# Optimization experiments

Hardware: AMD Instinct MI355X
Metric: run time of the kernel (lower is better)

Reference implementation:

```python
import jax, jax.numpy as jnp
import numpy as np

B, T, E, H, HD = 4, 1500, 1280, 20, 64
SCALING = HD ** -0.5


def setup_inputs() -> dict:
    key = jax.random.key(0)
    ks = jax.random.split(key, 8)
    s = 0.02
    return {
        "hidden_states": jax.random.normal(ks[0], (B, 1, T, E), jnp.float32),
        "attention_mask": jnp.zeros((B, 1, T, T), jnp.float32),
        "Wq": jax.random.normal(ks[1], (H, HD, E), jnp.float32) * s,
        "bq": jax.random.normal(ks[2], (H, HD), jnp.float32) * s,
        "Wk": jax.random.normal(ks[3], (H, HD, E), jnp.float32) * s,
        "Wv": jax.random.normal(ks[4], (H, HD, E), jnp.float32) * s,
        "bv": jax.random.normal(ks[5], (H, HD), jnp.float32) * s,
        "Wo": jax.random.normal(ks[6], (E, E), jnp.float32) * s,
        "bo": jax.random.normal(ks[7], (E,), jnp.float32) * s,
    }


def reference(hidden_states, attention_mask, Wq, bq, Wk, Wv, bv, Wo, bo):
    # hidden_states: [B, 1, T, E] (NHWC with H=1, as in the torch module)
    b, _, t, e = hidden_states.shape
    x = hidden_states[:, 0]  # [B, T, E]
    # Per-head 1x1 Conv2d projections == batched linear over stacked head weights.
    # Scaling is folded into q (the module bakes it into q_proj weights/bias).
    q = (jnp.einsum("bte,hde->bhtd", x, Wq) + bq[None, :, None, :]) * SCALING
    k = jnp.einsum("bse,hde->bhsd", x, Wk)
    v = jnp.einsum("bse,hde->bhsd", x, Wv) + bv[None, :, None, :]
    # attention_mask broadcasts over the head dim (module adds it per head as [B,1,T,S])
    scores = jnp.einsum("bhtd,bhsd->bhts", q, k) + attention_mask  # [B,H,T,S]
    attn = jax.nn.softmax(scores, axis=-1)
    out = jnp.einsum("bhts,bhsd->bhtd", attn, v)  # [B,H,T,HD]
    out = out.transpose(0, 2, 1, 3).reshape(b, t, e)  # concat heads on channel dim
    final = jnp.einsum("bte,fe->btf", out, Wo) + bo  # 1x1 Conv2d out_proj
    return final[:, None, :, :]  # [B,1,T,E]
```

## Files before the change

### kernel.cpp

```cpp
#include <hip/hip_runtime.h>

#define T_LEN 1500
#define TP    1536
#define EDIM  1280
#define NH    20
#define HD    64
#define KDIM  1280
#define NT    20

#define LOG2E 1.4426950408889634f

#define OFF_X    ((size_t)0)
#define OFF_AO   ((size_t)0)
#define OFF_W    ((size_t)7700480)
#define OFF_WO   ((size_t)12615680)
#define OFF_Q    ((size_t)14254080)
#define OFF_K    ((size_t)22118400)
#define OFF_VT   ((size_t)29982720)

typedef float  f32x4  __attribute__((ext_vector_type(4)));
typedef float  f32x16 __attribute__((ext_vector_type(16)));
typedef short  s16x8  __attribute__((ext_vector_type(8)));
typedef __bf16 bf16x8 __attribute__((ext_vector_type(8)));
typedef unsigned short u16;
typedef unsigned int   u32;
typedef unsigned int u32x4 __attribute__((ext_vector_type(4)));

__device__ __forceinline__ f32x4 mfma_bf16(s16x8 a, s16x8 b, f32x4 c) {
  return __builtin_amdgcn_mfma_f32_16x16x32_bf16(
      __builtin_bit_cast(bf16x8, a), __builtin_bit_cast(bf16x8, b), c, 0, 0, 0);
}

__device__ __forceinline__ f32x16 mfma32(s16x8 a, s16x8 b, f32x16 c) {
  return __builtin_amdgcn_mfma_f32_32x32x16_bf16(
      __builtin_bit_cast(bf16x8, a), __builtin_bit_cast(bf16x8, b), c, 0, 0, 0);
}

__device__ __forceinline__ u16 f2bf(float f) {
  union { float f; unsigned int u; } a; a.f = f;
  return (u16)((a.u + 0x7fffu + ((a.u >> 16) & 1u)) >> 16);
}

__device__ __forceinline__ float fexp2(float x) {
  return __builtin_amdgcn_exp2f(x);
}

__device__ __forceinline__ void gl_lds16(const u16* g, u16* l) {
  __builtin_amdgcn_global_load_lds(
      (const __attribute__((address_space(1))) unsigned int*)(const void*)g,
      (__attribute__((address_space(3))) unsigned int*)(void*)l, 16, 0, 0);
}


__global__ __launch_bounds__(256) void prep_kernel(
    const float* __restrict__ x, const float* __restrict__ wq,
    const float* __restrict__ wk, const float* __restrict__ wv,
    const float* __restrict__ wo, const float* __restrict__ mask,
    u16* __restrict__ ws, u32* __restrict__ nzflags) {
  const int S0 = 1925120;
  const int S1 = 1228800;
  const int S2 = 409600;
  const int P1 = 46080;
  const int S3 = 2250000;
  const int TOT = S0 + S1 + S2 + 3 * P1 + S3;
  for (int v = blockIdx.x * 256 + threadIdx.x; v < TOT; v += gridDim.x * 256) {
    if (v < S0) {
      int i = v * 4;
      int m = i / EDIM, e = i - m * EDIM;
      int ep = (e & ~63) | (((((e >> 3) & 7) ^ (m & 7))) << 3) | (e & 7);
      ushort4 o;
      if (m < 6000) {
        float4 f = *(const float4*)(x + i);
        o = make_ushort4(f2bf(f.x), f2bf(f.y), f2bf(f.z), f2bf(f.w));
      } else {
        o = make_ushort4(0, 0, 0, 0);
      }
      *(ushort4*)(ws + OFF_X + (size_t)m * EDIM + ep) = o;
    } else if (v < S0 + S1) {
      int j = (v - S0) * 4;
      int n = j / EDIM, e = j - n * EDIM;
      const float* s = (n < 1280) ? wq + (size_t)n * EDIM + e
                     : (n < 2560) ? wk + (size_t)(n - 1280) * EDIM + e
                                  : wv + (size_t)(n - 2560) * EDIM + e;
      float4 f = *(const float4*)s;
      int ep = (e & ~63) | (((((e >> 3) & 7) ^ (n & 7))) << 3) | (e & 7);
      *(ushort4*)(ws + OFF_W + (size_t)n * EDIM + ep) =
          make_ushort4(f2bf(f.x), f2bf(f.y), f2bf(f.z), f2bf(f.w));
    } else if (v < S0 + S1 + S2) {
      int j = (v - S0 - S1) * 4;
      int n = j / EDIM, e = j - n * EDIM;
      float4 f = *(const float4*)(wo + j);
      int ep = (e & ~63) | (((((e >> 3) & 7) ^ (n & 7))) << 3) | (e & 7);
      *(ushort4*)(ws + OFF_WO + (size_t)n * EDIM + ep) =
          make_ushort4(f2bf(f.x), f2bf(f.y), f2bf(f.z), f2bf(f.w));
    } else if (v < S0 + S1 + S2 + 3 * P1) {
      int p = v - (S0 + S1 + S2);
      ushort4 z = make_ushort4(0, 0, 0, 0);
      if (p < P1) {
        int p4 = p * 4; int bh = p4 / 2304; int rem = p4 - bh * 2304;
        int tt = rem >> 6, d = rem & 63;
        *(ushort4*)(ws + OFF_Q + ((size_t)(bh * TP + 1500 + tt)) * HD + d) = z;
      } else if (p < 2 * P1) {
        int p4 = (p - P1) * 4; int bh = p4 / 2304; int rem = p4 - bh * 2304;
        int tt = rem >> 6, d = rem & 63;
        *(ushort4*)(ws + OFF_K + ((size_t)(bh * TP + 1500 + tt)) * HD + d) = z;
      } else {
        int p4 = (p - 2 * P1) * 4; int bh = p4 / 2304; int rem = p4 - bh * 2304;
        int d = rem / 36, ss = rem - d * 36;
        int t = 1500 + ss;
        int tphys = (t & ~63) | (((((t >> 3) & 7) ^ (d & 7))) << 3) | (t & 7);
        *(ushort4*)(ws + OFF_VT + ((size_t)(bh * HD + d)) * TP + tphys) = z;
      }
    } else {
      int p = v - (S0 + S1 + S2 + 3 * P1);
      int i4 = p * 4;
      int bb = i4 / 2250000;
      int rem = i4 - bb * 2250000;
      int q = rem / 1500;
      int s = rem - q * 1500;
      float4 f = *(const float4*)(mask + (size_t)bb * 2250000 + rem);
      if (f.x != 0.f || f.y != 0.f || f.z != 0.f || f.w != 0.f)
        atomicOr(&nzflags[(bb * 12 + (q >> 7)) * 24 + (s >> 6)], 1u);
    }
  }
}

__device__ __forceinline__ void gemm_mainloop256(
    const u16* __restrict__ A, const u16* __restrict__ B,
    int mt, int nt, u16* lds, f32x4 acc[4][4]) {
  const int tid = threadIdx.x;
  const int lane = tid & 63, wid = tid >> 6;
  const int lg = lane >> 4, lr = lane & 15;
  const int wr = wid >> 1, wn = wid & 1;

  const u16* aB = A + (size_t)(mt * 256) * KDIM;
  const u16* bB = B + (size_t)(nt * 128) * KDIM;
  size_t aOff[4], bOff[2];
  #pragma unroll
  for (int l = 0; l < 4; ++l) {
    int gid = l * 512 + tid;
    aOff[l] = (size_t)(gid >> 3) * KDIM + (gid & 7) * 8;
  }
  #pragma unroll
  for (int l = 0; l < 2; ++l) {
    int gid = l * 512 + tid;
    bOff[l] = (size_t)(gid >> 3) * KDIM + (gid & 7) * 8;
  }
  const int ldsOff = tid * 8;
  int arow[4], brow[4];
  #pragma unroll
  for (int i = 0; i < 4; ++i) arow[i] = (wr * 64 + i * 16 + lr) * 64;
  #pragma unroll
  for (int j = 0; j < 4; ++j) brow[j] = (wn * 64 + j * 16 + lr) * 64;
  const int gsw0 = ((lg) ^ (lr & 7)) * 8;
  const int gsw1 = ((4 + lg) ^ (lr & 7)) * 8;

  #pragma unroll
  for (int t = 0; t < 2; ++t) {
    u16* dA = lds + t * 24576;
    u16* dB = dA + 16384;
    gl_lds16(aB + aOff[0] + t * 64, dA + ldsOff);
    gl_lds16(aB + aOff[1] + t * 64, dA + ldsOff + 4096);
    gl_lds16(bB + bOff[0] + t * 64, dB + ldsOff);
    gl_lds16(aB + aOff[2] + t * 64, dA + ldsOff + 8192);
    gl_lds16(aB + aOff[3] + t * 64, dA + ldsOff + 12288);
    gl_lds16(bB + bOff[1] + t * 64, dB + ldsOff + 4096);
  }
  asm volatile("s_waitcnt vmcnt(6)" ::: "memory");
  __builtin_amdgcn_s_barrier();
  __builtin_amdgcn_sched_barrier(0);
  s16x8 ca[4], cb[4];
  #pragma unroll
  for (int i = 0; i < 4; ++i) ca[i] = *(const s16x8*)(lds + arow[i] + gsw0);
  #pragma unroll
  for (int j = 0; j < 4; ++j) cb[j] = *(const s16x8*)(lds + 16384 + brow[j] + gsw0);

  int s = 0;
  #pragma unroll 1
  for (int kt = 0; kt < NT; ++kt) {
    u16* cA = lds + s * 24576;
    u16* cB = cA + 16384;
    int ssl = s + 2; if (ssl >= 3) ssl -= 3;
    u16* sA = lds + ssl * 24576;
    u16* sB = sA + 16384;
    const bool doStage = (kt + 2 < NT);
    if (doStage) {
      gl_lds16(aB + aOff[0] + (kt + 2) * 64, sA + ldsOff);
      gl_lds16(aB + aOff[1] + (kt + 2) * 64, sA + ldsOff + 4096);
      gl_lds16(bB + bOff[0] + (kt + 2) * 64, sB + ldsOff);
    }
    s16x8 na[4], nb[4];
    #pragma unroll
    for (int i = 0; i < 4; ++i) na[i] = *(const s16x8*)(cA + arow[i] + gsw1);
    #pragma unroll
    for (int j = 0; j < 4; ++j) nb[j] = *(const s16x8*)(cB + brow[j] + gsw1);
    __builtin_amdgcn_s_setprio(1);
    #pragma unroll
    for (int i = 0; i < 4; ++i)
      #pragma unroll
      for (int j = 0; j < 4; ++j)
        acc[i][j] = mfma_bf16(ca[i], cb[j], acc[i][j]);
    __builtin_amdgcn_s_setprio(0);
    if (doStage) {
      gl_lds16(aB + aOff[2] + (kt + 2) * 64, sA + ldsOff + 8192);
      gl_lds16(aB + aOff[3] + (kt + 2) * 64, sA + ldsOff + 12288);
      gl_lds16(bB + bOff[1] + (kt + 2) * 64, sB + ldsOff + 4096);
    }
    if (kt < NT - 1) {
      asm volatile("s_waitcnt lgkmcnt(0)" ::: "memory");
      if (kt < NT - 2) asm volatile("s_waitcnt vmcnt(6)" ::: "memory");
      else             asm volatile("s_waitcnt vmcnt(0)" ::: "memory");
      __builtin_amdgcn_s_barrier();
      __builtin_amdgcn_sched_barrier(0);
      int sn = s + 1; if (sn >= 3) sn = 0;
      const u16* nA = lds + sn * 24576;
      const u16* nB2 = nA + 16384;
      #pragma unroll
      for (int i = 0; i < 4; ++i) ca[i] = *(const s16x8*)(nA + arow[i] + gsw0);
      #pragma unroll
      for (int j = 0; j < 4; ++j) cb[j] = *(const s16x8*)(nB2 + brow[j] + gsw0);
    }
    __builtin_amdgcn_s_setprio(1);
    #pragma unroll
    for (int i = 0; i < 4; ++i)
      #pragma unroll
      for (int j = 0; j < 4; ++j)
        acc[i][j] = mfma_bf16(na[i], nb[j], acc[i][j]);
    __builtin_amdgcn_s_setprio(0);
    s = s + 1; if (s >= 3) s = 0;
  }
}

__global__ __launch_bounds__(512) void gemm_qkv_kernel(
    const u16* __restrict__ X, const u16* __restrict__ W,
    const float* __restrict__ bq, const float* __restrict__ bv,
    u16* __restrict__ Qw, u16* __restrict__ Kw, u16* __restrict__ Vtw) {
  __shared__ __align__(16) u16 lds[3 * 24576];
  const int bid = blockIdx.x;
  const int xcd = bid & 7, idx = bid >> 3;
  const int mt = xcd * 3 + idx % 3;
  const int nt = idx / 3;
  f32x4 acc[4][4] = {};
  gemm_mainloop256(X, W, mt, nt, lds, acc);
  const int tid = threadIdx.x;
  const int lane = tid & 63, wid = tid >> 6;
  const int lg = lane >> 4, lr = lane & 15;
  const int wr = wid >> 1, wn = wid & 1;
  #pragma unroll
  for (int i = 0; i < 4; ++i) {
    #pragma unroll
    for (int r = 0; r < 4; ++r) {
      int mm = mt * 256 + wr * 64 + i * 16 + lg * 4 + r;
      if (mm >= 6000) continue;
      int bt = mm / 1500, tt = mm - bt * 1500;
      #pragma unroll
      for (int j = 0; j < 4; ++j) {
        int n = nt * 128 + wn * 64 + j * 16 + lr;
        float v = acc[i][j][r];
        if (n < 1280) {
          int hh = n >> 6, d = n & 63;
          Qw[((size_t)(bt * NH + hh) * TP + tt) * HD + d] =
              f2bf((v + bq[n]) * (0.125f * LOG2E));
        } else if (n < 2560) {
          int nn = n - 1280, hh = nn >> 6, d = nn & 63;
          int dp = ((((d >> 3) ^ (tt & 7))) << 3) | (d & 7);
          Kw[((size_t)(bt * NH + hh) * TP + tt) * HD + dp] = f2bf(v);
        } else {
          int nn = n - 2560, hh = nn >> 6, d = nn & 63;
          int tphys = (tt & ~63) | (((((tt >> 3) & 7) ^ (d & 7))) << 3) | (tt & 7);
          Vtw[((size_t)(bt * NH + hh) * HD + d) * TP + tphys] = f2bf(v + bv[nn]);
        }
      }
    }
  }
}

__global__ __launch_bounds__(256) void attn_kernel(
    const u16* __restrict__ Qw, const u16* __restrict__ Kw,
    const u16* __restrict__ Vtw, const float* __restrict__ mask,
    const u32* __restrict__ nzflags, u16* __restrict__ AO) {
  __shared__ __align__(16) u16 Kb[2][64 * 64];
  __shared__ __align__(16) u16 Vb[2][64 * 64];
  const int bid = blockIdx.x;
  const int qt = bid / 80;
  const int bhid = bid % 80;
  const int bb = bhid / NH, hh = bhid % NH;
  const int tid = threadIdx.x;
  const int w = tid >> 6;
  const int lane = tid & 63;
  const int lq = lane & 31;
  const int hi = lane >> 5;
  const int q0 = qt * 128 + w * 32;
  const int qrow = q0 + lq;
  const int qm = qrow < (T_LEN - 1) ? qrow : (T_LEN - 1);
  const u16* Qp = Qw + (size_t)bhid * TP * HD;
  const u16* Kp = Kw + (size_t)bhid * TP * HD;
  const u16* Vp = Vtw + (size_t)bhid * HD * TP;
  const float* mp = mask + (size_t)bb * T_LEN * T_LEN + (size_t)qm * T_LEN;
  const u32* nzp = nzflags + (bb * 12 + qt) * 24;

  s16x8 qf[4];
  #pragma unroll
  for (int c = 0; c < 4; ++c)
    qf[c] = *(const s16x8*)(Qp + (size_t)qrow * HD + c * 16 + hi * 8);

  s16x8 ones;
  #pragma unroll
  for (int i = 0; i < 8; ++i) ones[i] = (short)0x3F80;

  f32x16 O0 = {}, O1 = {}, lacc = {};
  float m = -3e38f;

  {
    gl_lds16(Kp + tid * 8,                 Kb[0] + tid * 8);
    gl_lds16(Kp + 2048 + tid * 8,          Kb[0] + 2048 + tid * 8);
    int r = tid >> 3, g = tid & 7;
    gl_lds16(Vp + (size_t)r * TP + g * 8,          Vb[0] + tid * 8);
    gl_lds16(Vp + (size_t)(r + 32) * TP + g * 8,   Vb[0] + 2048 + tid * 8);
  }
  __syncthreads();

  int buf = 0;
  #pragma unroll 1
  for (int st = 0; st < 24; ++st) {
    const int s0 = st * 64;
    if (st < 23) {
      const int sn = s0 + 64;
      gl_lds16(Kp + (size_t)sn * HD + tid * 8,        Kb[buf ^ 1] + tid * 8);
      gl_lds16(Kp + (size_t)sn * HD + 2048 + tid * 8, Kb[buf ^ 1] + 2048 + tid * 8);
      int r = tid >> 3, g = tid & 7;
      gl_lds16(Vp + (size_t)r * TP + sn + g * 8,        Vb[buf ^ 1] + tid * 8);
      gl_lds16(Vp + (size_t)(r + 32) * TP + sn + g * 8, Vb[buf ^ 1] + 2048 + tid * 8);
    }
    const bool has_mask = nzp[st] != 0u;
    const u16* kb = Kb[buf];
    f32x16 S0a = {}, S1a = {};
    #pragma unroll
    for (int c = 0; c < 4; ++c) {
      int gc = 2 * c + hi;
      int gs = (gc ^ (lq & 7)) << 3;
      s16x8 k0 = *(const s16x8*)(kb + lq * 64 + gs);
      s16x8 k1 = *(const s16x8*)(kb + (32 + lq) * 64 + gs);
      S0a = mfma32(k0, qf[c], S0a);
      S1a = mfma32(k1, qf[c], S1a);
    }
    float p[32];
    #pragma unroll
    for (int r = 0; r < 16; ++r) { p[r] = S0a[r]; p[16 + r] = S1a[r]; }
    if (has_mask) {
      f32x4 mk[2][4];
      #pragma unroll
      for (int sh = 0; sh < 2; ++sh)
        #pragma unroll
        for (int g = 0; g < 4; ++g) {
          int sb = s0 + sh * 32 + 8 * g + 4 * hi;
          if (sb > T_LEN - 4) sb = T_LEN - 4;
          mk[sh][g] = *(const f32x4*)(mp + sb);
        }
      #pragma unroll
      for (int r = 0; r < 16; ++r) {
        p[r]      = fmaf(mk[0][r >> 2][r & 3], LOG2E, p[r]);
        p[16 + r] = fmaf(mk[1][r >> 2][r & 3], LOG2E, p[16 + r]);
      }
    }
    if (st == 23) {
      if (hi) { p[12] = p[13] = p[14] = p[15] = -1e30f; }
      #pragma unroll
      for (int r = 16; r < 32; ++r) p[r] = -1e30f;
    }
    float t1[16];
    #pragma unroll
    for (int r = 0; r < 16; ++r) t1[r] = fmaxf(p[r], p[r + 16]);
    #pragma unroll
    for (int r = 0; r < 8; ++r) t1[r] = fmaxf(t1[r], t1[r + 8]);
    float mx = fmaxf(fmaxf(fmaxf(t1[0], t1[1]), fmaxf(t1[2], t1[3])),
                     fmaxf(fmaxf(t1[4], t1[5]), fmaxf(t1[6], t1[7])));
    mx = fmaxf(mx, __shfl_xor(mx, 32));
    if (!__all(mx <= m + 8.f)) {
      float mn = fmaxf(m, mx);
      float sc = fexp2(m - mn);
      O0 *= sc; O1 *= sc; lacc *= sc;
      m = mn;
    }
    #pragma unroll
    for (int r = 0; r < 32; ++r) p[r] = fexp2(p[r] - m);
    const u16* vb = Vb[buf];
    #pragma unroll
    for (int sh = 0; sh < 2; ++sh) {
      u32 pk[8];
      #pragma unroll
      for (int j = 0; j < 8; ++j)
        asm("v_cvt_pk_bf16_f32 %0, %1, %2"
            : "=v"(pk[j]) : "v"(p[sh * 16 + 2 * j]), "v"(p[sh * 16 + 2 * j + 1]));
      asm("v_permlane32_swap_b32 %0, %1" : "+v"(pk[0]), "+v"(pk[2]));
      asm("v_permlane32_swap_b32 %0, %1" : "+v"(pk[1]), "+v"(pk[3]));
      asm("v_permlane32_swap_b32 %0, %1" : "+v"(pk[4]), "+v"(pk[6]));
      asm("v_permlane32_swap_b32 %0, %1" : "+v"(pk[5]), "+v"(pk[7]));
      u32x4 ta = {pk[0], pk[1], pk[2], pk[3]};
      u32x4 tb = {pk[4], pk[5], pk[6], pk[7]};
      s16x8 pfa = __builtin_bit_cast(s16x8, ta);
      s16x8 pfb = __builtin_bit_cast(s16x8, tb);
      lacc = mfma32(ones, pfa, lacc);
      lacc = mfma32(ones, pfb, lacc);
      int ga = sh * 4 + hi, gb = sh * 4 + 2 + hi;
      {
        int d = lq;
        s16x8 va = *(const s16x8*)(vb + d * 64 + ((ga ^ (d & 7)) << 3));
        s16x8 vc = *(const s16x8*)(vb + d * 64 + ((gb ^ (d & 7)) << 3));
        O0 = mfma32(va, pfa, O0);
        O0 = mfma32(vc, pfb, O0);
      }
      {
        int d = 32 + lq;
        s16x8 va = *(const s16x8*)(vb + d * 64 + ((ga ^ (d & 7)) << 3));
        s16x8 vc = *(const s16x8*)(vb + d * 64 + ((gb ^ (d & 7)) << 3));
        O1 = mfma32(va, pfa, O1);
        O1 = mfma32(vc, pfb, O1);
      }
    }
    __syncthreads();
    buf ^= 1;
  }

  if (qrow < T_LEN) {
    float inv = 1.f / lacc[0];
    int arow = bb * T_LEN + qrow;
    int key = arow & 7;
    size_t base = (size_t)arow * EDIM + hh * 64;
    #pragma unroll
    for (int g = 0; g < 4; ++g) {
      ushort4 o0, o1;
      o0.x = f2bf(O0[4 * g + 0] * inv); o0.y = f2bf(O0[4 * g + 1] * inv);
      o0.z = f2bf(O0[4 * g + 2] * inv); o0.w = f2bf(O0[4 * g + 3] * inv);
      o1.x = f2bf(O1[4 * g + 0] * inv); o1.y = f2bf(O1[4 * g + 1] * inv);
      o1.z = f2bf(O1[4 * g + 2] * inv); o1.w = f2bf(O1[4 * g + 3] * inv);
      *(ushort4*)(AO + base + ((g ^ key) << 3) + 4 * hi)       = o0;
      *(ushort4*)(AO + base + (((4 + g) ^ key) << 3) + 4 * hi) = o1;
    }
  }
}

__global__ __launch_bounds__(512) void gemm_out_kernel(
    const u16* __restrict__ AOb, const u16* __restrict__ Wob,
    const float* __restrict__ bo, float* __restrict__ out) {
  __shared__ __align__(16) u16 lds[3 * 24576];
  const int bid = blockIdx.x;
  const int xcd = bid & 7, idx = bid >> 3;
  const int mt = xcd * 3 + idx % 3;
  const int nt = idx / 3;
  f32x4 acc[4][4] = {};
  gemm_mainloop256(AOb, Wob, mt, nt, lds, acc);
  const int tid = threadIdx.x;
  const int lane = tid & 63, wid = tid >> 6;
  const int lg = lane >> 4, lr = lane & 15;
  const int wr = wid >> 1, wn = wid & 1;
  #pragma unroll
  for (int i = 0; i < 4; ++i) {
    #pragma unroll
    for (int r = 0; r < 4; ++r) {
      int mm = mt * 256 + wr * 64 + i * 16 + lg * 4 + r;
      if (mm >= 6000) continue;
      #pragma unroll
      for (int j = 0; j < 4; ++j) {
        int n = nt * 128 + wn * 64 + j * 16 + lr;
        out[(size_t)mm * EDIM + n] = acc[i][j][r] + bo[n];
      }
    }
  }
}

extern "C" void kernel_launch(void* const* d_in, const int* in_sizes, int n_in,
                              void* d_out, int out_size, void* d_ws, size_t ws_size,
                              hipStream_t stream) {
  const float* x    = (const float*)d_in[0];
  const float* mask = (const float*)d_in[1];
  const float* wq   = (const float*)d_in[2];
  const float* bq   = (const float*)d_in[3];
  const float* wk   = (const float*)d_in[4];
  const float* wv   = (const float*)d_in[5];
  const float* bv   = (const float*)d_in[6];
  const float* wo   = (const float*)d_in[7];
  const float* bo   = (const float*)d_in[8];
  float* out = (float*)d_out;
  u16* ws = (u16*)d_ws;
  u32* nzflags = (u32*)d_out;

  hipMemsetAsync(nzflags, 0, 1152 * sizeof(u32), stream);
  prep_kernel<<<2048, 256, 0, stream>>>(x, wq, wk, wv, wo, mask, ws, nzflags);
  gemm_qkv_kernel<<<720, 512, 0, stream>>>(
      ws + OFF_X, ws + OFF_W, bq, bv, ws + OFF_Q, ws + OFF_K, ws + OFF_VT);
  attn_kernel<<<960, 256, 0, stream>>>(
      ws + OFF_Q, ws + OFF_K, ws + OFF_VT, mask, nzflags, ws + OFF_AO);
  gemm_out_kernel<<<240, 512, 0, stream>>>(
      ws + OFF_AO, ws + OFF_WO, bo, out);
}
```

Baseline: 242.4 us.

## Use 256x256 square tiles with double-buffered mainloop for QKV GEMM

Replaces the 256x128 triple-buffered QKV GEMM mainloop with a 256x256 tile, 8 waves arranged 2x4, each computing 128x64 with a two-stage LDS double buffer. The grid is halved to 360 blocks, raising arithmetic intensity per loaded byte. The trade-offs are more accumulator registers (128 floats per thread), fewer blocks than CUs (a possible load imbalance), and a shallower prefetch pipeline with a full barrier each k-step.

```diff
diff --git a/kernel.cpp b/kernel.cpp
--- a/kernel.cpp
+++ b/kernel.cpp
@@ -125,6 +125,90 @@
   }
 }
 
+__device__ __forceinline__ void gemm_mainloop256sq(
+    const u16* __restrict__ A, const u16* __restrict__ B,
+    int mt, int nt, u16* lds, f32x4 acc[8][4]) {
+  const int tid = threadIdx.x;
+  const int lane = tid & 63, wid = tid >> 6;
+  const int lg = lane >> 4, lr = lane & 15;
+  const int wr = wid >> 2, wn = wid & 3;
+
+  const u16* aB = A + (size_t)(mt * 256) * KDIM;
+  const u16* bB = B + (size_t)(nt * 256) * KDIM;
+  size_t off[4];
+  #pragma unroll
+  for (int l = 0; l < 4; ++l) {
+    int gid = l * 512 + tid;
+    off[l] = (size_t)(gid >> 3) * KDIM + (gid & 7) * 8;
+  }
+  const int ldsOff = tid * 8;
+  int arow[8], brow[4];
+  #pragma unroll
+  for (int i = 0; i < 8; ++i) arow[i] = (wr * 128 + i * 16 + lr) * 64;
+  #pragma unroll
+  for (int j = 0; j < 4; ++j) brow[j] = 16384 + (wn * 64 + j * 16 + lr) * 64;
+  const int gsw0 = ((lg) ^ (lr & 7)) * 8;
+  const int gsw1 = ((4 + lg) ^ (lr & 7)) * 8;
+
+  #pragma unroll
+  for (int l = 0; l < 4; ++l) gl_lds16(aB + off[l], lds + ldsOff + l * 4096);
+  #pragma unroll
+  for (int l = 0; l < 4; ++l) gl_lds16(bB + off[l], lds + 16384 + ldsOff + l * 4096);
+  asm volatile("s_waitcnt vmcnt(0)" ::: "memory");
+  __builtin_amdgcn_s_barrier();
+  __builtin_amdgcn_sched_barrier(0);
+
+  int s = 0;
+  #pragma unroll 1
+  for (int kt = 0; kt < NT; ++kt) {
+    const u16* cur = lds + s * 32768;
+    u16* nxt = lds + (s ^ 1) * 32768;
+    if (kt + 1 < NT) {
+      #pragma unroll
+      for (int l = 0; l < 4; ++l)
+        gl_lds16(aB + off[l] + (kt + 1) * 64, nxt + ldsOff + l * 4096);
+      #pragma unroll
+      for (int l = 0; l < 4; ++l)
+        gl_lds16(bB + off[l] + (kt + 1) * 64, nxt + 16384 + ldsOff + l * 4096);
+    }
+    {
+      s16x8 af[8], bf[4];
+      #pragma unroll
+      for (int i = 0; i < 8; ++i) af[i] = *(const s16x8*)(cur + arow[i] + gsw0);
+      #pragma unroll
+      for (int j = 0; j < 4; ++j) bf[j] = *(const s16x8*)(cur + brow[j] + gsw0);
+      __builtin_amdgcn_s_setprio(1);
+      #pragma unroll
+      for (int i = 0; i < 8; ++i)
+        #pragma unroll
+        for (int j = 0; j < 4; ++j)
+          acc[i][j] = mfma_bf16(af[i], bf[j], acc[i][j]);
+      __builtin_amdgcn_s_setprio(0);
+    }
+    {
+      s16x8 af[8], bf[4];
+      #pragma unroll
+      for (int i = 0; i < 8; ++i) af[i] = *(const s16x8*)(cur + arow[i] + gsw1);
+      #pragma unroll
+      for (int j = 0; j < 4; ++j) bf[j] = *(const s16x8*)(cur + brow[j] + gsw1);
+      __builtin_amdgcn_s_setprio(1);
+      #pragma unroll
+      for (int i = 0; i < 8; ++i)
+        #pragma unroll
+        for (int j = 0; j < 4; ++j)
+          acc[i][j] = mfma_bf16(af[i], bf[j], acc[i][j]);
+      __builtin_amdgcn_s_setprio(0);
+    }
+    if (kt < NT - 1) {
+      asm volatile("s_waitcnt lgkmcnt(0)" ::: "memory");
+      asm volatile("s_waitcnt vmcnt(0)" ::: "memory");
+      __builtin_amdgcn_s_barrier();
+      __builtin_amdgcn_sched_barrier(0);
+    }
+    s ^= 1;
+  }
+}
+
 __device__ __forceinline__ void gemm_mainloop256(
     const u16* __restrict__ A, const u16* __restrict__ B,
     int mt, int nt, u16* lds, f32x4 acc[4][4]) {
@@ -231,31 +315,31 @@
   }
 }
 
-__global__ __launch_bounds__(512) void gemm_qkv_kernel(
+__global__ __launch_bounds__(512, 2) void gemm_qkv_kernel(
     const u16* __restrict__ X, const u16* __restrict__ W,
     const float* __restrict__ bq, const float* __restrict__ bv,
     u16* __restrict__ Qw, u16* __restrict__ Kw, u16* __restrict__ Vtw) {
-  __shared__ __align__(16) u16 lds[3 * 24576];
+  __shared__ __align__(16) u16 lds[2 * 32768];
   const int bid = blockIdx.x;
   const int xcd = bid & 7, idx = bid >> 3;
   const int mt = xcd * 3 + idx % 3;
   const int nt = idx / 3;
-  f32x4 acc[4][4] = {};
-  gemm_mainloop256(X, W, mt, nt, lds, acc);
+  f32x4 acc[8][4] = {};
+  gemm_mainloop256sq(X, W, mt, nt, lds, acc);
   const int tid = threadIdx.x;
   const int lane = tid & 63, wid = tid >> 6;
   const int lg = lane >> 4, lr = lane & 15;
-  const int wr = wid >> 1, wn = wid & 1;
-  #pragma unroll
-  for (int i = 0; i < 4; ++i) {
+  const int wr = wid >> 2, wn = wid & 3;
+  #pragma unroll
+  for (int i = 0; i < 8; ++i) {
     #pragma unroll
     for (int r = 0; r < 4; ++r) {
-      int mm = mt * 256 + wr * 64 + i * 16 + lg * 4 + r;
+      int mm = mt * 256 + wr * 128 + i * 16 + lg * 4 + r;
       if (mm >= 6000) continue;
       int bt = mm / 1500, tt = mm - bt * 1500;
       #pragma unroll
       for (int j = 0; j < 4; ++j) {
-        int n = nt * 128 + wn * 64 + j * 16 + lr;
+        int n = nt * 256 + wn * 64 + j * 16 + lr;
         float v = acc[i][j][r];
         if (n < 1280) {
           int hh = n >> 6, d = n & 63;
@@ -487,7 +571,7 @@
 
   hipMemsetAsync(nzflags, 0, 1152 * sizeof(u32), stream);
   prep_kernel<<<2048, 256, 0, stream>>>(x, wq, wk, wv, wo, mask, ws, nzflags);
-  gemm_qkv_kernel<<<720, 512, 0, stream>>>(
+  gemm_qkv_kernel<<<360, 512, 0, stream>>>(
       ws + OFF_X, ws + OFF_W, bq, bv, ws + OFF_Q, ws + OFF_K, ws + OFF_VT);
   attn_kernel<<<960, 256, 0, stream>>>(
       ws + OFF_Q, ws + OFF_K, ws + OFF_VT, mask, nzflags, ws + OFF_AO);
```

New measurement: 255.3 us. 1.05x slower.
